# Kernel optimization log

Hardware: AMD Instinct MI355X
Metric: run time of the kernel (lower is better)

## Reference

```python
import jax, jax.numpy as jnp
import numpy as np

B, S, E = 8, 2048, 2048   # batch, items, embedding_width
H, Dh = 16, 128           # head_width, head_embeddings (E = H*Dh)
M = 1024                  # memory_width


def setup_inputs() -> dict:
    key = jax.random.key(0)
    ks = jax.random.split(key, 9)
    scale_e = 1.0 / np.sqrt(E)
    scale_d = 1.0 / np.sqrt(Dh)
    return {
        "tensor": jax.random.normal(ks[0], (B, S, E), dtype=jnp.float32),
        # Query: Linear(E -> [H, Dh])
        "Wq": jax.random.normal(ks[1], (E, H, Dh), dtype=jnp.float32) * scale_e,
        "bq": jnp.zeros((H, Dh), dtype=jnp.float32),
        # trainable key/value banks + calibration (kaiming-uniform-like init)
        "key_params": (jax.random.uniform(ks[2], (H, M, Dh), dtype=jnp.float32) * 2 - 1) * np.sqrt(6.0 / Dh),
        "calibration": jnp.zeros((H, M, Dh), dtype=jnp.float32),
        "value": (jax.random.uniform(ks[3], (H, M, Dh), dtype=jnp.float32) * 2 - 1) * np.sqrt(6.0 / Dh),
        # Dehead: Linear([H, Dh] -> E)
        "Wd": jax.random.normal(ks[4], (H, Dh, E), dtype=jnp.float32) * scale_d,
        "bd": jnp.zeros((E,), dtype=jnp.float32),
    }


def reference(tensor, Wq, bq, key_params, calibration, value, Wd, bd):
    # query projection to heads: (B,S,E) -> (B,H,S,Dh) (fuses transpose(-2,-3))
    q = jnp.einsum("bse,ehd->bhsd", tensor, Wq) + bq[:, None, :]
    # eval-mode dropout is identity; key = KeyParameters + CalibrationBuffer
    k = key_params + calibration                      # (H,M,Dh)
    # scores scaled by sqrt(FULL embedding width), per the source
    score = jnp.einsum("bhsd,hmd->bhsm", q, k) / jnp.sqrt(jnp.float32(E))
    attn = jax.nn.softmax(score, axis=-1)             # (B,H,S,M)
    out = jnp.einsum("bhsm,hmd->bhsd", attn, value)   # (B,H,S,Dh)
    # dehead: (B,H,S,Dh) -> (B,S,E)
    return jnp.einsum("bhsd,hde->bse", out, Wd) + bd
```

## Files before the change

kernel.cpp:

```cpp
#include <hip/hip_runtime.h>
#include <stdint.h>

#define B_ 8
#define S_ 2048
#define E_ 2048
#define H_ 16
#define DH_ 128
#define M_ 1024
#define K_ 2048

typedef float f32x4 __attribute__((ext_vector_type(4)));
typedef __bf16 bf16x8 __attribute__((ext_vector_type(8)));
typedef unsigned short ushort8 __attribute__((ext_vector_type(8)));
typedef unsigned short ushort4v __attribute__((ext_vector_type(4)));
typedef float float4v __attribute__((ext_vector_type(4)));

static __device__ __forceinline__ unsigned short f2bf(float f) {
  unsigned int u = __builtin_bit_cast(unsigned int, f);
  u += 0x7fffu + ((u >> 16) & 1u);
  return (unsigned short)(u >> 16);
}

static __device__ __forceinline__ float exp2f_fast(float x) {
#if __has_builtin(__builtin_amdgcn_exp2f)
  return __builtin_amdgcn_exp2f(x);
#else
  return __expf(x * 0.6931471805599453f);
#endif
}

static __device__ __forceinline__ f32x4 mfma16(ushort8 a, ushort8 b, f32x4 c) {
  return __builtin_amdgcn_mfma_f32_16x16x32_bf16(
      __builtin_bit_cast(bf16x8, a), __builtin_bit_cast(bf16x8, b), c, 0, 0, 0);
}

static __device__ __forceinline__ void gload_lds16(const void* g, void* l) {
  __builtin_amdgcn_global_load_lds(
      (const __attribute__((address_space(1))) unsigned int*)g,
      (__attribute__((address_space(3))) unsigned int*)l, 16, 0, 0);
}


__global__ void cvt_bf16(const float* __restrict__ in, unsigned short* __restrict__ out, int n4) {
  int i = blockIdx.x * blockDim.x + threadIdx.x;
  int stride = gridDim.x * blockDim.x;
  for (; i < n4; i += stride) {
    float4v v = ((const float4v*)in)[i];
    ushort4v o;
    o[0] = f2bf(v[0]); o[1] = f2bf(v[1]); o[2] = f2bf(v[2]); o[3] = f2bf(v[3]);
    ((ushort4v*)out)[i] = o;
  }
}

__global__ void addcvt_bf16(const float* __restrict__ a, const float* __restrict__ b,
                            unsigned short* __restrict__ out, int n4) {
  int i = blockIdx.x * blockDim.x + threadIdx.x;
  int stride = gridDim.x * blockDim.x;
  for (; i < n4; i += stride) {
    float4v va = ((const float4v*)a)[i];
    float4v vb = ((const float4v*)b)[i];
    ushort4v o;
    o[0] = f2bf(va[0] + vb[0]); o[1] = f2bf(va[1] + vb[1]);
    o[2] = f2bf(va[2] + vb[2]); o[3] = f2bf(va[3] + vb[3]);
    ((ushort4v*)out)[i] = o;
  }
}

__global__ __launch_bounds__(256) void transpose_cvt(const float* __restrict__ in,
                                                     unsigned short* __restrict__ out,
                                                     int R, int C) {
  __shared__ float t[64][65];
  const int tx = threadIdx.x & 63, ty = threadIdx.x >> 6;
  const size_t base = (size_t)blockIdx.z * R * C;
  const int r0 = blockIdx.y * 64, c0 = blockIdx.x * 64;
#pragma unroll
  for (int i = 0; i < 64; i += 4)
    t[i + ty][tx] = in[base + (size_t)(r0 + i + ty) * C + (c0 + tx)];
  __syncthreads();
#pragma unroll
  for (int i = 0; i < 64; i += 4)
    out[base + (size_t)(c0 + i + ty) * R + (r0 + tx)] = f2bf(t[tx][i + ty]);
}

template <int EPI>
__global__ __launch_bounds__(512, 2) void gemm8p(const unsigned short* __restrict__ A,
                                                 const unsigned short* __restrict__ BT,
                                                 const float* __restrict__ bias,
                                                 void* __restrict__ Cout) {
  __shared__ __align__(16) unsigned short a_lds[2][2][8192];
  __shared__ __align__(16) unsigned short b_lds[2][2][8192];
  const int tid = threadIdx.x;
  const int w = tid >> 6, lane = tid & 63;
  const int l16 = lane & 15, l4 = lane >> 4;
  const int wr = w >> 2, wc = w & 3;
  const int bid = blockIdx.x;
  const int n0 = (bid & 7) << 8;
  const int m0 = (bid >> 3) << 8;

  const int rp0 = tid >> 3, gg0 = tid & 7, s0 = gg0 ^ (rp0 & 7);
  const int srow = rp0 * 2 + (s0 >> 2), sg = s0 & 3;
  const unsigned short* pA = A + (size_t)(m0 + srow) * K_ + sg * 8;
  const unsigned short* pB = BT + (size_t)(n0 + srow) * K_ + sg * 8;
  const int laneG = ((l16 >> 1) * 8 + (((l16 & 1) * 4 + l4) ^ ((l16 >> 1) & 7))) * 8;

  f32x4 acc[8][4];
#pragma unroll
  for (int i = 0; i < 8; ++i)
#pragma unroll
    for (int j = 0; j < 4; ++j) acc[i][j] = (f32x4)(0.f);

  ushort8 aF[4], bF[4];

#define STG(dst, srcp, T, kh)                                                \
  do {                                                                       \
    const unsigned short* s_ = (srcp) + (T) * 64 + (kh) * 32;                \
    gload_lds16(s_, &(dst)[tid * 8]);                                        \
    gload_lds16(s_ + (size_t)128 * K_, &(dst)[(512 + tid) * 8]);             \
  } while (0)

#define LDA(mg, buf, ks)                                                     \
  do {                                                                       \
    _Pragma("unroll") for (int mf = 0; mf < 4; ++mf)                         \
      aF[mf] = *(const ushort8*)&a_lds[buf][ks]                              \
          [(wr * 512 + ((mg) * 4 + mf) * 64) * 8 + laneG];                   \
  } while (0)

#define LDB(buf, ks)                                                         \
  do {                                                                       \
    _Pragma("unroll") for (int nf = 0; nf < 4; ++nf)                         \
      bF[nf] = *(const ushort8*)&b_lds[buf][ks]                              \
          [(wc * 256 + nf * 64) * 8 + laneG];                                \
  } while (0)

#define MM(mg)                                                               \
  do {                                                                       \
    __builtin_amdgcn_s_setprio(1);                                           \
    _Pragma("unroll") for (int mf = 0; mf < 4; ++mf)                         \
      _Pragma("unroll") for (int nf = 0; nf < 4; ++nf)                       \
        acc[(mg) * 4 + mf][nf] = mfma16(aF[mf], bF[nf], acc[(mg) * 4 + mf][nf]); \
    __builtin_amdgcn_s_setprio(0);                                           \
  } while (0)

#define NOVM ((void)0)
#define VMC6 asm volatile("s_waitcnt vmcnt(6)" ::: "memory")
#define VMC0 asm volatile("s_waitcnt vmcnt(0)" ::: "memory")

#define PHASE(mg, ks, buf, LOADB, STAGE, VM)                                 \
  do {                                                                       \
    if (LOADB) { LDB(buf, ks); }                                             \
    LDA(mg, buf, ks);                                                        \
    STAGE;                                                                   \
    __builtin_amdgcn_s_barrier();                                            \
    asm volatile("s_waitcnt lgkmcnt(0)" ::: "memory");                       \
    __builtin_amdgcn_sched_barrier(0);                                       \
    MM(mg);                                                                  \
    VM;                                                                      \
    __builtin_amdgcn_s_barrier();                                            \
  } while (0)

  STG(a_lds[0][0], pA, 0, 0);
  STG(b_lds[0][0], pB, 0, 0);
  STG(a_lds[0][1], pA, 0, 1);
  STG(b_lds[0][1], pB, 0, 1);
  STG(b_lds[1][0], pB, 1, 0);
  STG(a_lds[1][0], pA, 1, 0);
  STG(b_lds[1][1], pB, 1, 1);
  __builtin_amdgcn_sched_barrier(0);
  VMC6;
  __builtin_amdgcn_s_barrier();
  __builtin_amdgcn_sched_barrier(0);

#pragma unroll 1
  for (int i = 0; i < 15; ++i) {
    const int t1 = 2 * i + 1, t2 = 2 * i + 2, t3 = 2 * i + 3;
    PHASE(0, 0, 0, 1, STG(a_lds[1][1], pA, t1, 1), NOVM);
    PHASE(1, 0, 0, 0, STG(b_lds[0][0], pB, t2, 0), NOVM);
    PHASE(1, 1, 0, 1, STG(a_lds[0][0], pA, t2, 0), NOVM);
    PHASE(0, 1, 0, 0, STG(b_lds[0][1], pB, t2, 1), VMC6);
    PHASE(0, 0, 1, 1, STG(a_lds[0][1], pA, t2, 1), NOVM);
    PHASE(1, 0, 1, 0, STG(b_lds[1][0], pB, t3, 0), NOVM);
    PHASE(1, 1, 1, 1, STG(a_lds[1][0], pA, t3, 0), NOVM);
    PHASE(0, 1, 1, 0, STG(b_lds[1][1], pB, t3, 1), VMC6);
  }
  PHASE(0, 0, 0, 1, STG(a_lds[1][1], pA, 31, 1), NOVM);
  PHASE(1, 0, 0, 0, NOVM, NOVM);
  PHASE(1, 1, 0, 1, NOVM, NOVM);
  PHASE(0, 1, 0, 0, NOVM, VMC0);
  PHASE(0, 0, 1, 1, NOVM, NOVM);
  PHASE(1, 0, 1, 0, NOVM, NOVM);
  PHASE(1, 1, 1, 1, NOVM, NOVM);
  PHASE(0, 1, 1, 0, NOVM, NOVM);

#undef PHASE
#undef STG
#undef LDA
#undef LDB
#undef MM

#pragma unroll
  for (int mf = 0; mf < 8; ++mf) {
    const int mb = m0 + wr * 128 + mf * 16 + l4 * 4;
#pragma unroll
    for (int nf = 0; nf < 4; ++nf) {
      const int n = n0 + wc * 64 + nf * 16 + l16;
      const float bv = bias[n];
#pragma unroll
      for (int r = 0; r < 4; ++r) {
        const float v = acc[mf][nf][r] + bv;
        const int m = mb + r;
        if (EPI == 0) {
          const int b = m >> 11, s = m & 2047, h = n >> 7, d = n & 127;
          ((unsigned short*)Cout)[(((size_t)(b * 16 + h) << 11) + s) * 128 + d] =
              f2bf(v * 0.031879358f);
        } else {
          ((float*)Cout)[(size_t)m * E_ + n] = v;
        }
      }
    }
  }
}

__global__ __launch_bounds__(256) void attn_kernel(const unsigned short* __restrict__ Qb,
                                                   const unsigned short* __restrict__ Kb,
                                                   const unsigned short* __restrict__ VT,
                                                   unsigned short* __restrict__ Ob) {
  const int bh = blockIdx.x, b = bh >> 4, h = bh & 15;
  const int s0 = blockIdx.y << 7;
  const int tid = threadIdx.x, w = tid >> 6, lane = tid & 63;
  const int l16 = lane & 15, l4 = lane >> 4;
  const int sw = s0 + w * 32;

  __shared__ __align__(16) unsigned short k_sm[2][32 * 128];
  __shared__ __align__(16) unsigned short v_sm[2][128 * 32];
  __shared__ __align__(16) unsigned short p_lds[4][32][40];

  const unsigned short* Kh = Kb + (size_t)h * M_ * DH_;
  const unsigned short* Vh = VT + (size_t)h * DH_ * M_;

  ushort8 aq[2][4];
  {
    const unsigned short* Qbase = Qb + ((size_t)(b * 16 + h) * S_ + sw) * DH_;
#pragma unroll
    for (int rb = 0; rb < 2; ++rb) {
      const unsigned short* qrow = Qbase + (size_t)(rb * 16 + l16) * DH_ + l4 * 8;
#pragma unroll
      for (int kk = 0; kk < 4; ++kk) aq[rb][kk] = *(const ushort8*)(qrow + kk * 32);
    }
  }

  float lsum[2][4];
  f32x4 o_acc[2][8];
#pragma unroll
  for (int rb = 0; rb < 2; ++rb) {
#pragma unroll
    for (int r = 0; r < 4; ++r) lsum[rb][r] = 0.f;
#pragma unroll
    for (int nc = 0; nc < 8; ++nc) o_acc[rb][nc] = (f32x4)(0.f);
  }

#define STAGE(bufidx, mc_)                                                              \
  do {                                                                                  \
    const int m0s = (mc_) << 5;                                                         \
    unsigned short* kdst = &k_sm[bufidx][0];                                            \
    unsigned short* vdst = &v_sm[bufidx][0];                                            \
    _Pragma("unroll") for (int i_ = 0; i_ < 2; ++i_) {                                  \
      const int g_ = i_ * 256 + tid;                                                    \
      const int kr = g_ >> 4, kc = g_ & 15;                                             \
      gload_lds16(Kh + (size_t)(m0s + kr) * DH_ + ((kc ^ (kr & 7)) << 3), kdst + g_ * 8); \
      const int vd = g_ >> 2, vc = g_ & 3;                                              \
      gload_lds16(Vh + (size_t)vd * M_ + m0s + ((vc ^ (vd & 3)) << 3), vdst + g_ * 8);  \
    }                                                                                   \
  } while (0)

  int cur = 0;
  STAGE(0, 0);
  __syncthreads();

  for (int mc = 0; mc < 32; ++mc) {
    if (mc < 31) STAGE(cur ^ 1, mc + 1);

    f32x4 sa[2][2];
#pragma unroll
    for (int rb = 0; rb < 2; ++rb)
#pragma unroll
      for (int nc = 0; nc < 2; ++nc) sa[rb][nc] = (f32x4)(0.f);

    __builtin_amdgcn_s_setprio(1);
#pragma unroll
    for (int nc = 0; nc < 2; ++nc) {
      const int row = nc * 16 + l16;
      const unsigned short* kbase = &k_sm[cur][row * DH_];
#pragma unroll
      for (int kk = 0; kk < 4; ++kk) {
        const int gran = (kk * 4 + l4) ^ (row & 7);
        ushort8 bk = *(const ushort8*)(kbase + gran * 8);
        sa[0][nc] = mfma16(aq[0][kk], bk, sa[0][nc]);
        sa[1][nc] = mfma16(aq[1][kk], bk, sa[1][nc]);
      }
    }
    __builtin_amdgcn_s_setprio(0);

#pragma unroll
    for (int rb = 0; rb < 2; ++rb) {
#pragma unroll
      for (int r = 0; r < 4; ++r) {
        const float p0 = exp2f_fast(sa[rb][0][r]);
        const float p1 = exp2f_fast(sa[rb][1][r]);
        lsum[rb][r] += p0 + p1;
        unsigned pu;
        asm("v_cvt_pk_bf16_f32 %0, %1, %2" : "=v"(pu) : "v"(p0), "v"(p1));
        unsigned paddr = (unsigned)(size_t)&p_lds[w][rb * 16 + l4 * 4 + r][l16];
        asm volatile("ds_write_b16 %0, %1\n\t"
                     "ds_write_b16_d16_hi %0, %1 offset:32"
                     :: "v"(paddr), "v"(pu) : "memory");
      }
    }

    ushort8 pf[2];
#pragma unroll
    for (int rb = 0; rb < 2; ++rb)
      pf[rb] = *(const ushort8*)&p_lds[w][rb * 16 + l16][l4 * 8];
    __builtin_amdgcn_s_setprio(1);
#pragma unroll
    for (int nc = 0; nc < 8; ++nc) {
      const int row = nc * 16 + l16;
      const int gran = l4 ^ (row & 3);
      ushort8 bv = *(const ushort8*)&v_sm[cur][row * 32 + gran * 8];
      o_acc[0][nc] = mfma16(pf[0], bv, o_acc[0][nc]);
      o_acc[1][nc] = mfma16(pf[1], bv, o_acc[1][nc]);
    }
    __builtin_amdgcn_s_setprio(0);

    __syncthreads();
    cur ^= 1;
  }
#undef STAGE

#pragma unroll
  for (int rb = 0; rb < 2; ++rb)
#pragma unroll
    for (int r = 0; r < 4; ++r) {
      float s = lsum[rb][r];
      s += __shfl_xor(s, 1, 64);
      s += __shfl_xor(s, 2, 64);
      s += __shfl_xor(s, 4, 64);
      s += __shfl_xor(s, 8, 64);
      const float inv = 1.0f / s;
      const int srow = sw + rb * 16 + l4 * 4 + r;
      unsigned short* orow = Ob + ((size_t)b * S_ + srow) * (H_ * DH_) + h * DH_;
#pragma unroll
      for (int nc = 0; nc < 8; ++nc)
        orow[nc * 16 + l16] = f2bf(o_acc[rb][nc][r] * inv);
    }
}


extern "C" void kernel_launch(void* const* d_in, const int* in_sizes, int n_in,
                              void* d_out, int out_size, void* d_ws, size_t ws_size,
                              hipStream_t stream) {
  const float* X   = (const float*)d_in[0];
  const float* Wq  = (const float*)d_in[1];
  const float* bq  = (const float*)d_in[2];
  const float* Kp  = (const float*)d_in[3];
  const float* Cal = (const float*)d_in[4];
  const float* V   = (const float*)d_in[5];
  const float* Wd  = (const float*)d_in[6];
  const float* bd  = (const float*)d_in[7];

  char* ws = (char*)d_ws;
  unsigned short* Xbf = (unsigned short*)(ws + 0);
  unsigned short* Ob  = Xbf;
  unsigned short* Qb  = (unsigned short*)(ws + 67108864);
  unsigned short* WqT = (unsigned short*)(ws + 134217728);
  unsigned short* WdT = (unsigned short*)(ws + 142606336);
  unsigned short* Kb  = (unsigned short*)(ws + 150994944);
  unsigned short* VT  = (unsigned short*)(ws + 155189248);

  cvt_bf16<<<2048, 256, 0, stream>>>(X, Xbf, (B_ * S_ * E_) / 4);
  addcvt_bf16<<<1024, 256, 0, stream>>>(Kp, Cal, Kb, (H_ * M_ * DH_) / 4);
  transpose_cvt<<<dim3(E_ / 64, E_ / 64, 1), 256, 0, stream>>>(Wq, WqT, E_, H_ * DH_);
  transpose_cvt<<<dim3(E_ / 64, E_ / 64, 1), 256, 0, stream>>>(Wd, WdT, H_ * DH_, E_);
  transpose_cvt<<<dim3(DH_ / 64, M_ / 64, H_), 256, 0, stream>>>(V, VT, M_, DH_);

  gemm8p<0><<<dim3(512), 512, 0, stream>>>(Xbf, WqT, bq, Qb);

  attn_kernel<<<dim3(B_ * H_, S_ / 128), 256, 0, stream>>>(Qb, Kb, VT, Ob);

  gemm8p<1><<<dim3(512), 512, 0, stream>>>(Ob, WdT, bd, (float*)d_out);
}
```

Baseline: 510.6 us.

## Rewrite attention kernel with 32x32 MFMA and register-resident probabilities

Replaces the 16x16x32 MFMA attention kernel with a 32x32x16 version. It computes transposed scores (K as A operand), so the exp'd probabilities can be packed into the PV operand using v_permlane32_swap instead of round-tripping through LDS. The kernel also uses 512-thread blocks over 256 query rows and 64-key chunks with double-buffered K/V staging. The aim is fewer MFMA issues, removal of the P LDS traffic, and larger reuse per staged tile. The cost is higher register pressure from 16-wide accumulators and a new reduction of the softmax sum through LDS. The final inv_lds write is read by other lanes without a barrier, which may be a correctness risk.

```diff
diff --git a/kernel.cpp b/kernel.cpp
--- a/kernel.cpp
+++ b/kernel.cpp
@@ -10,9 +10,11 @@
 #define K_ 2048
 
 typedef float f32x4 __attribute__((ext_vector_type(4)));
+typedef float f32x16 __attribute__((ext_vector_type(16)));
 typedef __bf16 bf16x8 __attribute__((ext_vector_type(8)));
 typedef unsigned short ushort8 __attribute__((ext_vector_type(8)));
 typedef unsigned short ushort4v __attribute__((ext_vector_type(4)));
+typedef unsigned int uint4v __attribute__((ext_vector_type(4)));
 typedef float float4v __attribute__((ext_vector_type(4)));
 
 static __device__ __forceinline__ unsigned short f2bf(float f) {
@@ -31,6 +33,11 @@
 
 static __device__ __forceinline__ f32x4 mfma16(ushort8 a, ushort8 b, f32x4 c) {
   return __builtin_amdgcn_mfma_f32_16x16x32_bf16(
+      __builtin_bit_cast(bf16x8, a), __builtin_bit_cast(bf16x8, b), c, 0, 0, 0);
+}
+
+static __device__ __forceinline__ f32x16 mfma32(ushort8 a, ushort8 b, f32x16 c) {
+  return __builtin_amdgcn_mfma_f32_32x32x16_bf16(
       __builtin_bit_cast(bf16x8, a), __builtin_bit_cast(bf16x8, b), c, 0, 0, 0);
 }
 
@@ -220,138 +227,133 @@
   }
 }
 
-__global__ __launch_bounds__(256) void attn_kernel(const unsigned short* __restrict__ Qb,
-                                                   const unsigned short* __restrict__ Kb,
-                                                   const unsigned short* __restrict__ VT,
-                                                   unsigned short* __restrict__ Ob) {
+__global__ __launch_bounds__(512, 2) void attn32(const unsigned short* __restrict__ Qb,
+                                                 const unsigned short* __restrict__ Kb,
+                                                 const unsigned short* __restrict__ VT,
+                                                 unsigned short* __restrict__ Ob) {
   const int bh = blockIdx.x, b = bh >> 4, h = bh & 15;
-  const int s0 = blockIdx.y << 7;
-  const int tid = threadIdx.x, w = tid >> 6, lane = tid & 63;
-  const int l16 = lane & 15, l4 = lane >> 4;
-  const int sw = s0 + w * 32;
-
-  __shared__ __align__(16) unsigned short k_sm[2][32 * 128];
-  __shared__ __align__(16) unsigned short v_sm[2][128 * 32];
-  __shared__ __align__(16) unsigned short p_lds[4][32][40];
+  const int tid = threadIdx.x, wv = tid >> 6, lane = tid & 63;
+  const int l32 = lane & 31, hi = lane >> 5;
+  const int s_glob = blockIdx.y * 256 + wv * 32 + l32;
+
+  __shared__ __align__(16) unsigned short k_sm[2][64 * 128];
+  __shared__ __align__(16) unsigned short v_sm[2][128 * 64];
+  __shared__ float inv_lds[8][32];
 
   const unsigned short* Kh = Kb + (size_t)h * M_ * DH_;
   const unsigned short* Vh = VT + (size_t)h * DH_ * M_;
 
-  ushort8 aq[2][4];
+  ushort8 qf[8];
   {
-    const unsigned short* Qbase = Qb + ((size_t)(b * 16 + h) * S_ + sw) * DH_;
-#pragma unroll
-    for (int rb = 0; rb < 2; ++rb) {
-      const unsigned short* qrow = Qbase + (size_t)(rb * 16 + l16) * DH_ + l4 * 8;
-#pragma unroll
-      for (int kk = 0; kk < 4; ++kk) aq[rb][kk] = *(const ushort8*)(qrow + kk * 32);
+    const unsigned short* qrow = Qb + ((size_t)(b * 16 + h) * S_ + s_glob) * DH_ + hi * 8;
+#pragma unroll
+    for (int dc = 0; dc < 8; ++dc) qf[dc] = *(const ushort8*)(qrow + dc * 16);
+  }
+
+  f32x16 oacc[4];
+#pragma unroll
+  for (int dt = 0; dt < 4; ++dt) oacc[dt] = (f32x16)(0.f);
+  float lsum = 0.f;
+
+#define ASTAGE(buf, ch)                                                        \
+  do {                                                                         \
+    const int m0_ = (ch) << 6;                                                 \
+    _Pragma("unroll") for (int j_ = 0; j_ < 2; ++j_) {                         \
+      const int t_ = j_ * 512 + tid;                                           \
+      const int m_ = t_ >> 4, p_ = t_ & 15;                                    \
+      gload_lds16(Kh + (size_t)(m0_ + m_) * DH_ + ((p_ ^ (m_ & 7)) << 3),      \
+                  &k_sm[buf][t_ * 8]);                                         \
+    }                                                                          \
+    _Pragma("unroll") for (int j_ = 0; j_ < 2; ++j_) {                         \
+      const int t_ = j_ * 512 + tid;                                           \
+      const int d_ = t_ >> 3, p_ = t_ & 7;                                     \
+      gload_lds16(Vh + (size_t)d_ * M_ + m0_ + ((p_ ^ (d_ & 7)) << 3),         \
+                  &v_sm[buf][t_ * 8]);                                         \
+    }                                                                          \
+  } while (0)
+
+  int cur = 0;
+  ASTAGE(0, 0);
+  __syncthreads();
+
+  for (int c = 0; c < 16; ++c) {
+    if (c < 15) ASTAGE(cur ^ 1, c + 1);
+
+    f32x16 sacc[2];
+    sacc[0] = (f32x16)(0.f);
+    sacc[1] = (f32x16)(0.f);
+#pragma unroll
+    for (int mb = 0; mb < 2; ++mb) {
+      const int m_ = mb * 32 + l32;
+      const unsigned short* kr = &k_sm[cur][m_ * 128];
+      __builtin_amdgcn_s_setprio(1);
+#pragma unroll
+      for (int dc = 0; dc < 8; ++dc) {
+        ushort8 kf = *(const ushort8*)(kr + (((dc * 2 + hi) ^ (m_ & 7)) << 3));
+        sacc[mb] = mfma32(kf, qf[dc], sacc[mb]);
+      }
+      __builtin_amdgcn_s_setprio(0);
     }
-  }
-
-  float lsum[2][4];
-  f32x4 o_acc[2][8];
-#pragma unroll
-  for (int rb = 0; rb < 2; ++rb) {
-#pragma unroll
-    for (int r = 0; r < 4; ++r) lsum[rb][r] = 0.f;
-#pragma unroll
-    for (int nc = 0; nc < 8; ++nc) o_acc[rb][nc] = (f32x4)(0.f);
-  }
-
-#define STAGE(bufidx, mc_)                                                              \
-  do {                                                                                  \
-    const int m0s = (mc_) << 5;                                                         \
-    unsigned short* kdst = &k_sm[bufidx][0];                                            \
-    unsigned short* vdst = &v_sm[bufidx][0];                                            \
-    _Pragma("unroll") for (int i_ = 0; i_ < 2; ++i_) {                                  \
-      const int g_ = i_ * 256 + tid;                                                    \
-      const int kr = g_ >> 4, kc = g_ & 15;                                             \
-      gload_lds16(Kh + (size_t)(m0s + kr) * DH_ + ((kc ^ (kr & 7)) << 3), kdst + g_ * 8); \
-      const int vd = g_ >> 2, vc = g_ & 3;                                              \
-      gload_lds16(Vh + (size_t)vd * M_ + m0s + ((vc ^ (vd & 3)) << 3), vdst + g_ * 8);  \
-    }                                                                                   \
-  } while (0)
-
-  int cur = 0;
-  STAGE(0, 0);
-  __syncthreads();
-
-  for (int mc = 0; mc < 32; ++mc) {
-    if (mc < 31) STAGE(cur ^ 1, mc + 1);
-
-    f32x4 sa[2][2];
-#pragma unroll
-    for (int rb = 0; rb < 2; ++rb)
-#pragma unroll
-      for (int nc = 0; nc < 2; ++nc) sa[rb][nc] = (f32x4)(0.f);
-
-    __builtin_amdgcn_s_setprio(1);
-#pragma unroll
-    for (int nc = 0; nc < 2; ++nc) {
-      const int row = nc * 16 + l16;
-      const unsigned short* kbase = &k_sm[cur][row * DH_];
-#pragma unroll
-      for (int kk = 0; kk < 4; ++kk) {
-        const int gran = (kk * 4 + l4) ^ (row & 7);
-        ushort8 bk = *(const ushort8*)(kbase + gran * 8);
-        sa[0][nc] = mfma16(aq[0][kk], bk, sa[0][nc]);
-        sa[1][nc] = mfma16(aq[1][kk], bk, sa[1][nc]);
+
+#pragma unroll
+    for (int mb = 0; mb < 2; ++mb) {
+      float pe[16];
+#pragma unroll
+      for (int r = 0; r < 16; ++r) {
+        pe[r] = exp2f_fast(sacc[mb][r]);
+        lsum += pe[r];
+      }
+      ushort8 pa[2];
+#pragma unroll
+      for (int mk = 0; mk < 2; ++mk) {
+        const int o = mk * 8;
+        unsigned x0, x1, y0, y1;
+        asm("v_cvt_pk_bf16_f32 %0, %1, %2" : "=v"(x0) : "v"(pe[o + 0]), "v"(pe[o + 1]));
+        asm("v_cvt_pk_bf16_f32 %0, %1, %2" : "=v"(x1) : "v"(pe[o + 2]), "v"(pe[o + 3]));
+        asm("v_cvt_pk_bf16_f32 %0, %1, %2" : "=v"(y0) : "v"(pe[o + 4]), "v"(pe[o + 5]));
+        asm("v_cvt_pk_bf16_f32 %0, %1, %2" : "=v"(y1) : "v"(pe[o + 6]), "v"(pe[o + 7]));
+        asm("v_permlane32_swap_b32 %0, %1" : "+v"(x0), "+v"(y0));
+        asm("v_permlane32_swap_b32 %0, %1" : "+v"(x1), "+v"(y1));
+        uint4v pw;
+        pw[0] = x0; pw[1] = x1; pw[2] = y0; pw[3] = y1;
+        pa[mk] = __builtin_bit_cast(ushort8, pw);
+      }
+#pragma unroll
+      for (int dt = 0; dt < 4; ++dt) {
+        const int d_ = dt * 32 + l32;
+        const unsigned short* vr = &v_sm[cur][d_ * 64];
+        __builtin_amdgcn_s_setprio(1);
+#pragma unroll
+        for (int mk = 0; mk < 2; ++mk) {
+          const int gv = mb * 4 + mk * 2 + hi;
+          ushort8 vf = *(const ushort8*)(vr + ((gv ^ (d_ & 7)) << 3));
+          oacc[dt] = mfma32(pa[mk], vf, oacc[dt]);
+        }
+        __builtin_amdgcn_s_setprio(0);
       }
     }
-    __builtin_amdgcn_s_setprio(0);
-
-#pragma unroll
-    for (int rb = 0; rb < 2; ++rb) {
-#pragma unroll
-      for (int r = 0; r < 4; ++r) {
-        const float p0 = exp2f_fast(sa[rb][0][r]);
-        const float p1 = exp2f_fast(sa[rb][1][r]);
-        lsum[rb][r] += p0 + p1;
-        unsigned pu;
-        asm("v_cvt_pk_bf16_f32 %0, %1, %2" : "=v"(pu) : "v"(p0), "v"(p1));
-        unsigned paddr = (unsigned)(size_t)&p_lds[w][rb * 16 + l4 * 4 + r][l16];
-        asm volatile("ds_write_b16 %0, %1\n\t"
-                     "ds_write_b16_d16_hi %0, %1 offset:32"
-                     :: "v"(paddr), "v"(pu) : "memory");
-      }
-    }
-
-    ushort8 pf[2];
-#pragma unroll
-    for (int rb = 0; rb < 2; ++rb)
-      pf[rb] = *(const ushort8*)&p_lds[w][rb * 16 + l16][l4 * 8];
-    __builtin_amdgcn_s_setprio(1);
-#pragma unroll
-    for (int nc = 0; nc < 8; ++nc) {
-      const int row = nc * 16 + l16;
-      const int gran = l4 ^ (row & 3);
-      ushort8 bv = *(const ushort8*)&v_sm[cur][row * 32 + gran * 8];
-      o_acc[0][nc] = mfma16(pf[0], bv, o_acc[0][nc]);
-      o_acc[1][nc] = mfma16(pf[1], bv, o_acc[1][nc]);
-    }
-    __builtin_amdgcn_s_setprio(0);
-
     __syncthreads();
     cur ^= 1;
   }
-#undef STAGE
-
-#pragma unroll
-  for (int rb = 0; rb < 2; ++rb)
-#pragma unroll
-    for (int r = 0; r < 4; ++r) {
-      float s = lsum[rb][r];
-      s += __shfl_xor(s, 1, 64);
-      s += __shfl_xor(s, 2, 64);
-      s += __shfl_xor(s, 4, 64);
-      s += __shfl_xor(s, 8, 64);
-      const float inv = 1.0f / s;
-      const int srow = sw + rb * 16 + l4 * 4 + r;
-      unsigned short* orow = Ob + ((size_t)b * S_ + srow) * (H_ * DH_) + h * DH_;
-#pragma unroll
-      for (int nc = 0; nc < 8; ++nc)
-        orow[nc * 16 + l16] = f2bf(o_acc[rb][nc][r] * inv);
+#undef ASTAGE
+
+  float tot = lsum + __shfl_xor(lsum, 32, 64);
+  if (hi == 0) inv_lds[wv][l32] = 1.0f / tot;
+#pragma unroll
+  for (int r = 0; r < 16; ++r) {
+    const int srow = (r & 3) + 8 * (r >> 2) + 4 * hi;
+    const float iv = inv_lds[wv][srow];
+    unsigned short* orow =
+        Ob + ((size_t)b * S_ + (size_t)(blockIdx.y * 256 + wv * 32 + srow)) * (H_ * DH_) +
+        h * DH_ + l32;
+#pragma unroll
+    for (int dt = 0; dt < 4; ++dt) {
+      const float val = oacc[dt][r] * iv;
+      unsigned u;
+      asm("v_cvt_pk_bf16_f32 %0, %1, %2" : "=v"(u) : "v"(val), "v"(val));
+      orow[dt * 32] = (unsigned short)u;
     }
+  }
 }
 
 
@@ -384,7 +386,7 @@
 
   gemm8p<0><<<dim3(512), 512, 0, stream>>>(Xbf, WqT, bq, Qb);
 
-  attn_kernel<<<dim3(B_ * H_, S_ / 128), 256, 0, stream>>>(Qb, Kb, VT, Ob);
+  attn32<<<dim3(B_ * H_, S_ / 256), 512, 0, stream>>>(Qb, Kb, VT, Ob);
 
   gemm8p<1><<<dim3(512), 512, 0, stream>>>(Ob, WdT, bd, (float*)d_out);
 }
```

Result: faster. 475.2 us (median of 2 runs) (-6.9%).
